# Optimization experiments

Hardware: AMD Instinct MI355X
Metric: run time of the kernel (lower is better)

## Reference

```python
import jax, jax.numpy as jnp
import numpy as np
import itertools

EPS = 1e-6
OUT = 1024            # out_size[0]
RRNG = (16.0, 16.0)   # local sampling region per column (rrange)


def setup_inputs() -> dict:
    key = jax.random.key(0)
    ks = jax.random.split(key, 6)
    b, n, c, g, rad, rank = 8, 4096, 32, 4, 4, 2
    k = n // c
    in_size = 1024
    rng = jnp.array([float(OUT), float(in_size)])
    # continuous index tuples, strictly inside [0, dim-1)
    means = jax.random.uniform(ks[0], (b, n, rank)) * (rng - 1.0)
    sigmas = jax.random.uniform(ks[1], (b, n, rank)) * 0.5 + 0.1
    values = jax.random.normal(ks[2], (b, n))
    x = jax.random.normal(ks[3], (b, in_size))
    sampled_u = jax.random.uniform(ks[4], (b, k, c, g, rank))
    rr_u = jax.random.uniform(ks[5], (b, k, c, rad, rank))
    return {"x": x, "means": means, "sigmas": sigmas, "values": values,
            "sampled_u": sampled_u, "rr_u": rr_u}


def _generate_integer_tuples(means, sampled_u, rr_u, rng, rrng):
    # means: (b,k,c,rank)
    b, k, c, rank = means.shape
    # floor/ceil combinatorics: itertools.product([True, False], repeat=rank)
    fm = jnp.asarray([[int(v) for v in bits]
                      for bits in itertools.product([True, False], repeat=rank)],
                     dtype=bool)                       # (2^rank, rank)
    m = means[:, :, :, None, :]                         # (b,k,c,1,rank)
    neighbor = jnp.where(fm[None, None, None], jnp.floor(m), jnp.ceil(m))
    neighbor = jnp.broadcast_to(neighbor, (b, k, c, 2 ** rank, rank)).astype(jnp.int32)
    # global uniform samples over the full index range
    sampled = jnp.floor(sampled_u * (1.0 - EPS) * rng).astype(jnp.int32)
    # local uniform samples in a window of size rrng around round(means)
    mns = jnp.round(means)[:, :, :, None, :]
    lower = mns - rrng * 0.5
    upper = mns + rrng * 0.5
    lower = jnp.where(lower < 0.0, 0.0, lower)
    lower = jnp.where(upper > rng, rng - rrng, lower)
    rr = jnp.floor(rr_u * (1.0 - EPS) * rrng + lower).astype(jnp.int32)
    allints = jnp.concatenate([neighbor, sampled, rr], axis=3)  # (b,k,c,L,rank)
    return allints.reshape(b, k, -1, rank)                      # l = c*L


def _densities(points, means, sigmas):
    # points: (b,k,l,rank)  means/sigmas: (b,k,c,rank) -> (b,k,l,c)
    inv = jnp.sqrt(1.0 / (EPS + sigmas))
    diff = (points[:, :, :, None, :] - means[:, :, None, :, :]) * inv[:, :, None, :, :]
    return jnp.exp(-0.5 * jnp.sum(diff * diff, axis=-1))


def _mark_dups(ids):
    # ids: (b,k,l) scalar-encoded tuples; True = later occurrence of a duplicate
    # within the same (b,k) chunk context. Stable sort keeps first occurrence.
    order = jnp.argsort(ids, axis=-1)
    s = jnp.take_along_axis(ids, order, axis=-1)
    dup_s = jnp.concatenate([jnp.zeros(s.shape[:-1] + (1,), dtype=bool),
                             s[..., 1:] == s[..., :-1]], axis=-1)
    inv = jnp.argsort(order, axis=-1)
    return jnp.take_along_axis(dup_s, inv, axis=-1)


def reference(x, means, sigmas, values, sampled_u, rr_u):
    b, n, rank = means.shape
    _, k, c, g, _ = sampled_u.shape
    in_size = x.shape[1]
    rng = jnp.array([OUT, in_size], dtype=x.dtype)
    rrng = jnp.array(RRNG, dtype=x.dtype)

    means = means.reshape(b, k, c, rank)
    sigmas = sigmas.reshape(b, k, c, rank)
    values = values.reshape(b, k, c)

    ints = _generate_integer_tuples(means, sampled_u, rr_u, rng, rrng)  # (b,k,l,rank)
    indfl = ints.astype(x.dtype)

    dups = _mark_dups(ints[..., 0] * in_size + ints[..., 1])            # (b,k,l)
    props = _densities(indfl, means, sigmas)                            # (b,k,l,c)
    props = jnp.where(dups[..., None], 0.0, props)
    props = props / jnp.sum(props, axis=2, keepdims=True)

    vals = jnp.sum(props * values[:, :, None, :], axis=3)               # (b,k,l)

    idx = ints.reshape(b, -1, rank)
    v = vals.reshape(b, -1)
    bidx = jnp.arange(b)[:, None]
    # sparse contraction: out[b, i0] += v * x[b, i1]
    contrib = v * x[bidx, idx[..., 1]]
    out = jnp.zeros((b, OUT), x.dtype).at[bidx, idx[..., 0]].add(contrib)
    return out
```

## Files before the change

### kernel.cpp

```cpp
#include <hip/hip_runtime.h>

#define CQ 32
#define KQ 128
#define NPTS 384
#define OUTN 1024
#define BQ 8
#define NACC (BQ * OUTN)
#define HSZ 1024
#define GPB 2
#define KB (KQ / GPB)
#define WS_NEED ((size_t)BQ * KB * OUTN * sizeof(float))

__global__ void zero_out(float* __restrict__ out) {
    int i = blockIdx.x * blockDim.x + threadIdx.x;
    if (i < NACC) out[i] = 0.0f;
}

__device__ __forceinline__ float wave_red_dpp(float v) {
#define DPPADD(ctrl)                                                              \
    {                                                                             \
        int t_ = __builtin_amdgcn_update_dpp(0, __float_as_int(v), (ctrl), 0xF,   \
                                             0xF, true);                          \
        v += __int_as_float(t_);                                                  \
    }
    DPPADD(0x111)
    DPPADD(0x112)
    DPPADD(0x114)
    DPPADD(0x118)
    DPPADD(0x142)
    DPPADD(0x143)
#undef DPPADD
    return v;
}

__global__ __launch_bounds__(NPTS) void sparse_part(
    const float* __restrict__ x,
    const float* __restrict__ means,
    const float* __restrict__ sigmas,
    const float* __restrict__ values,
    const float* __restrict__ su,
    const float* __restrict__ ru,
    float* __restrict__ dst,
    int use_ws)
{
    const int kb = blockIdx.x, b = blockIdx.y;
    const int tid = threadIdx.x;
    const int lane = tid & 63, wid = tid >> 6;

    __shared__ float m0s[CQ], m1s[CQ], i0s[CQ], i1s[CQ], valc[CQ];
    __shared__ int htab[HSZ];
    __shared__ float part[6][CQ];
    __shared__ float wnorm[CQ];
    __shared__ float acc[OUTN];

    if (use_ws) {
        for (int i = tid; i < OUTN; i += NPTS) acc[i] = 0.0f;
    }

    const int c = tid / 12, j = tid % 12;
    const float CEPS = (float)(1.0 - 1e-6);

    for (int g = 0; g < GPB; ++g) {
        const int k = kb * GPB + g;
        const int gk = b * KQ + k;

        for (int i = tid; i < HSZ; i += NPTS) htab[i] = -1;
        if (tid < CQ) {
            int cb = gk * CQ + tid;
            m0s[tid] = means[cb * 2 + 0];
            m1s[tid] = means[cb * 2 + 1];
            i0s[tid] = __fsqrt_rn(__fdiv_rn(1.0f, __fadd_rn(1e-6f, sigmas[cb * 2 + 0])));
            i1s[tid] = __fsqrt_rn(__fdiv_rn(1.0f, __fadd_rn(1e-6f, sigmas[cb * 2 + 1])));
            valc[tid] = values[cb];
        }
        __syncthreads();

        const int cb = gk * CQ + c;
        const float mm0 = m0s[c], mm1 = m1s[c];
        int p0, p1;
        if (j < 4) {
            p0 = (int)((j >= 2) ? ceilf(mm0) : floorf(mm0));
            p1 = (int)((j & 1) ? ceilf(mm1) : floorf(mm1));
        } else if (j < 8) {
            int ub = (cb * 4 + (j - 4)) * 2;
            float u0 = su[ub], u1 = su[ub + 1];
            p0 = (int)floorf(__fmul_rn(__fmul_rn(u0, CEPS), 1024.0f));
            p1 = (int)floorf(__fmul_rn(__fmul_rn(u1, CEPS), 1024.0f));
        } else {
            int ub = (cb * 4 + (j - 8)) * 2;
            float u0 = ru[ub], u1 = ru[ub + 1];
            float mn0 = rintf(mm0), mn1 = rintf(mm1);
            float lo0 = mn0 - 8.0f; if (lo0 < 0.0f) lo0 = 0.0f; if (mn0 + 8.0f > 1024.0f) lo0 = 1008.0f;
            float lo1 = mn1 - 8.0f; if (lo1 < 0.0f) lo1 = 0.0f; if (mn1 + 8.0f > 1024.0f) lo1 = 1008.0f;
            p0 = (int)floorf(__fadd_rn(__fmul_rn(__fmul_rn(u0, CEPS), 16.0f), lo0));
            p1 = (int)floorf(__fadd_rn(__fmul_rn(__fmul_rn(u1, CEPS), 16.0f), lo1));
        }

        const int myid = p0 * 1024 + p1;
        int slot = (int)(((unsigned)myid * 2654435761u) >> 22);
        bool dup = false;
        while (true) {
            int prev = atomicCAS(&htab[slot], -1, myid);
            if (prev == -1) break;
            if (prev == myid) { dup = true; break; }
            slot = (slot + 1) & (HSZ - 1);
        }

        const float pf0 = (float)p0, pf1 = (float)p1;
        float pr[CQ];
        #pragma unroll
        for (int cc = 0; cc < CQ; ++cc) {
            float d0 = (pf0 - m0s[cc]) * i0s[cc];
            float d1 = (pf1 - m1s[cc]) * i1s[cc];
            float e = __expf(-0.5f * (d0 * d0 + d1 * d1));
            pr[cc] = dup ? 0.0f : e;
        }

        #pragma unroll
        for (int cc = 0; cc < CQ; ++cc) {
            float v = wave_red_dpp(pr[cc]);
            if (lane == 63) part[wid][cc] = v;
        }
        __syncthreads();
        if (tid < CQ) {
            float s = 0.0f;
            #pragma unroll
            for (int w = 0; w < 6; ++w) s += part[w][tid];
            wnorm[tid] = valc[tid] / s;
        }
        __syncthreads();

        if (!dup) {
            float vals = 0.0f;
            #pragma unroll
            for (int cc = 0; cc < CQ; ++cc) vals += pr[cc] * wnorm[cc];
            int g1 = p1 < 0 ? 0 : (p1 > OUTN - 1 ? OUTN - 1 : p1);
            float contrib = vals * x[b * OUTN + g1];
            if (p0 >= 0 && p0 < OUTN) {
                if (use_ws) atomicAdd(&acc[p0], contrib);
                else        atomicAdd(&dst[b * OUTN + p0], contrib);
            }
        }
        __syncthreads();
    }

    if (use_ws) {
        float* w = dst + ((size_t)b * KB + kb) * OUTN;
        for (int i = tid; i < OUTN; i += NPTS) w[i] = acc[i];
    }
}

__global__ void reduce_ws(const float* __restrict__ ws, float* __restrict__ out) {
    int t = blockIdx.x * blockDim.x + threadIdx.x;
    if (t >= NACC) return;
    int b = t >> 10, cidx = t & (OUTN - 1);
    const float* p = ws + (size_t)b * KB * OUTN + cidx;
    float s0 = 0.0f, s1 = 0.0f, s2 = 0.0f, s3 = 0.0f;
    #pragma unroll
    for (int k = 0; k < KB; k += 4) {
        s0 += p[(size_t)(k + 0) * OUTN];
        s1 += p[(size_t)(k + 1) * OUTN];
        s2 += p[(size_t)(k + 2) * OUTN];
        s3 += p[(size_t)(k + 3) * OUTN];
    }
    out[t] = (s0 + s1) + (s2 + s3);
}

extern "C" void kernel_launch(void* const* d_in, const int* in_sizes, int n_in,
                              void* d_out, int out_size, void* d_ws, size_t ws_size,
                              hipStream_t stream) {
    const float* x      = (const float*)d_in[0];
    const float* means  = (const float*)d_in[1];
    const float* sigmas = (const float*)d_in[2];
    const float* values = (const float*)d_in[3];
    const float* su     = (const float*)d_in[4];
    const float* ru     = (const float*)d_in[5];
    float* out = (float*)d_out;
    float* ws  = (float*)d_ws;

    if (ws_size >= WS_NEED) {
        sparse_part<<<dim3(KB, BQ), dim3(NPTS), 0, stream>>>(
            x, means, sigmas, values, su, ru, ws, 1);
        reduce_ws<<<dim3((NACC + 127) / 128), dim3(128), 0, stream>>>(ws, out);
    } else {
        zero_out<<<dim3((NACC + 255) / 256), dim3(256), 0, stream>>>(out);
        sparse_part<<<dim3(KB, BQ), dim3(NPTS), 0, stream>>>(
            x, means, sigmas, values, su, ru, out, 0);
    }
}
```

Measured before the change: 91.86 us.

## Process one k-group per block and hoist global loads ahead of hash-table init

Each block now handles a single k-group instead of looping over two, doubling the grid to 1024 blocks. Global loads of means, sigmas, values and the sample tuples are issued at kernel start and overlap the hash-table and accumulator initialisation. Gaussian parameters are packed into a float4 in shared memory so each inner-loop iteration does one LDS read. The trade-off is a workspace twice as large, so the reduce kernel sums 128 partial rows per output instead of 64 and moves twice the data.

Measured after the change: 96.51 us. +5.1%, slower.

```diff
diff --git a/kernel.cpp b/kernel.cpp
--- a/kernel.cpp
+++ b/kernel.cpp
@@ -7,9 +7,7 @@
 #define BQ 8
 #define NACC (BQ * OUTN)
 #define HSZ 1024
-#define GPB 2
-#define KB (KQ / GPB)
-#define WS_NEED ((size_t)BQ * KB * OUTN * sizeof(float))
+#define WS_NEED ((size_t)BQ * KQ * OUTN * sizeof(float))
 
 __global__ void zero_out(float* __restrict__ out) {
     int i = blockIdx.x * blockDim.x + threadIdx.x;
@@ -43,109 +41,111 @@
     float* __restrict__ dst,
     int use_ws)
 {
-    const int kb = blockIdx.x, b = blockIdx.y;
+    const int k = blockIdx.x, b = blockIdx.y;
     const int tid = threadIdx.x;
     const int lane = tid & 63, wid = tid >> 6;
+    const int gk = b * KQ + k;
+    const int c = tid / 12, j = tid % 12;
+    const int cb = gk * CQ + c;
+    const float CEPS = (float)(1.0 - 1e-6);
 
-    __shared__ float m0s[CQ], m1s[CQ], i0s[CQ], i1s[CQ], valc[CQ];
+    __shared__ float4 gp[CQ];
+    __shared__ float valc[CQ];
     __shared__ int htab[HSZ];
     __shared__ float part[6][CQ];
     __shared__ float wnorm[CQ];
     __shared__ float acc[OUTN];
 
+    const float2 mcb = *(const float2*)&means[cb * 2];
+    float2 uu = make_float2(0.0f, 0.0f);
+    if (j >= 8)       uu = *(const float2*)&ru[(cb * 4 + (j - 8)) * 2];
+    else if (j >= 4)  uu = *(const float2*)&su[(cb * 4 + (j - 4)) * 2];
+    float2 mg, sg; float vv = 0.0f;
+    if (tid < CQ) {
+        int cbs = gk * CQ + tid;
+        mg = *(const float2*)&means[cbs * 2];
+        sg = *(const float2*)&sigmas[cbs * 2];
+        vv = values[cbs];
+    }
+
+    for (int i = tid; i < HSZ; i += NPTS) htab[i] = -1;
     if (use_ws) {
         for (int i = tid; i < OUTN; i += NPTS) acc[i] = 0.0f;
     }
+    if (tid < CQ) {
+        float i0 = __fsqrt_rn(__fdiv_rn(1.0f, __fadd_rn(1e-6f, sg.x)));
+        float i1 = __fsqrt_rn(__fdiv_rn(1.0f, __fadd_rn(1e-6f, sg.y)));
+        gp[tid] = make_float4(mg.x, mg.y, i0, i1);
+        valc[tid] = vv;
+    }
 
-    const int c = tid / 12, j = tid % 12;
-    const float CEPS = (float)(1.0 - 1e-6);
+    const float mm0 = mcb.x, mm1 = mcb.y;
+    int p0, p1;
+    if (j < 4) {
+        p0 = (int)((j >= 2) ? ceilf(mm0) : floorf(mm0));
+        p1 = (int)((j & 1) ? ceilf(mm1) : floorf(mm1));
+    } else if (j < 8) {
+        p0 = (int)floorf(__fmul_rn(__fmul_rn(uu.x, CEPS), 1024.0f));
+        p1 = (int)floorf(__fmul_rn(__fmul_rn(uu.y, CEPS), 1024.0f));
+    } else {
+        float mn0 = rintf(mm0), mn1 = rintf(mm1);
+        float lo0 = mn0 - 8.0f; if (lo0 < 0.0f) lo0 = 0.0f; if (mn0 + 8.0f > 1024.0f) lo0 = 1008.0f;
+        float lo1 = mn1 - 8.0f; if (lo1 < 0.0f) lo1 = 0.0f; if (mn1 + 8.0f > 1024.0f) lo1 = 1008.0f;
+        p0 = (int)floorf(__fadd_rn(__fmul_rn(__fmul_rn(uu.x, CEPS), 16.0f), lo0));
+        p1 = (int)floorf(__fadd_rn(__fmul_rn(__fmul_rn(uu.y, CEPS), 16.0f), lo1));
+    }
+    __syncthreads();
 
-    for (int g = 0; g < GPB; ++g) {
-        const int k = kb * GPB + g;
-        const int gk = b * KQ + k;
+    const int myid = p0 * 1024 + p1;
+    int slot = (int)(((unsigned)myid * 2654435761u) >> 22);
+    bool dup = false;
+    while (true) {
+        int prev = atomicCAS(&htab[slot], -1, myid);
+        if (prev == -1) break;
+        if (prev == myid) { dup = true; break; }
+        slot = (slot + 1) & (HSZ - 1);
+    }
 
-        for (int i = tid; i < HSZ; i += NPTS) htab[i] = -1;
-        if (tid < CQ) {
-            int cb = gk * CQ + tid;
-            m0s[tid] = means[cb * 2 + 0];
-            m1s[tid] = means[cb * 2 + 1];
-            i0s[tid] = __fsqrt_rn(__fdiv_rn(1.0f, __fadd_rn(1e-6f, sigmas[cb * 2 + 0])));
-            i1s[tid] = __fsqrt_rn(__fdiv_rn(1.0f, __fadd_rn(1e-6f, sigmas[cb * 2 + 1])));
-            valc[tid] = values[cb];
+    const float pf0 = (float)p0, pf1 = (float)p1;
+    float pr[CQ];
+    #pragma unroll
+    for (int cc = 0; cc < CQ; ++cc) {
+        float4 g = gp[cc];
+        float d0 = (pf0 - g.x) * g.z;
+        float d1 = (pf1 - g.y) * g.w;
+        float e = __expf(-0.5f * (d0 * d0 + d1 * d1));
+        pr[cc] = dup ? 0.0f : e;
+    }
+
+    #pragma unroll
+    for (int cc = 0; cc < CQ; ++cc) {
+        float v = wave_red_dpp(pr[cc]);
+        if (lane == 63) part[wid][cc] = v;
+    }
+    __syncthreads();
+    if (tid < CQ) {
+        float s = 0.0f;
+        #pragma unroll
+        for (int w = 0; w < 6; ++w) s += part[w][tid];
+        wnorm[tid] = valc[tid] / s;
+    }
+    __syncthreads();
+
+    if (!dup) {
+        float vals = 0.0f;
+        #pragma unroll
+        for (int cc = 0; cc < CQ; ++cc) vals += pr[cc] * wnorm[cc];
+        int g1 = p1 < 0 ? 0 : (p1 > OUTN - 1 ? OUTN - 1 : p1);
+        float contrib = vals * x[b * OUTN + g1];
+        if (p0 >= 0 && p0 < OUTN) {
+            if (use_ws) atomicAdd(&acc[p0], contrib);
+            else        atomicAdd(&dst[b * OUTN + p0], contrib);
         }
-        __syncthreads();
-
-        const int cb = gk * CQ + c;
-        const float mm0 = m0s[c], mm1 = m1s[c];
-        int p0, p1;
-        if (j < 4) {
-            p0 = (int)((j >= 2) ? ceilf(mm0) : floorf(mm0));
-            p1 = (int)((j & 1) ? ceilf(mm1) : floorf(mm1));
-        } else if (j < 8) {
-            int ub = (cb * 4 + (j - 4)) * 2;
-            float u0 = su[ub], u1 = su[ub + 1];
-            p0 = (int)floorf(__fmul_rn(__fmul_rn(u0, CEPS), 1024.0f));
-            p1 = (int)floorf(__fmul_rn(__fmul_rn(u1, CEPS), 1024.0f));
-        } else {
-            int ub = (cb * 4 + (j - 8)) * 2;
-            float u0 = ru[ub], u1 = ru[ub + 1];
-            float mn0 = rintf(mm0), mn1 = rintf(mm1);
-            float lo0 = mn0 - 8.0f; if (lo0 < 0.0f) lo0 = 0.0f; if (mn0 + 8.0f > 1024.0f) lo0 = 1008.0f;
-            float lo1 = mn1 - 8.0f; if (lo1 < 0.0f) lo1 = 0.0f; if (mn1 + 8.0f > 1024.0f) lo1 = 1008.0f;
-            p0 = (int)floorf(__fadd_rn(__fmul_rn(__fmul_rn(u0, CEPS), 16.0f), lo0));
-            p1 = (int)floorf(__fadd_rn(__fmul_rn(__fmul_rn(u1, CEPS), 16.0f), lo1));
-        }
-
-        const int myid = p0 * 1024 + p1;
-        int slot = (int)(((unsigned)myid * 2654435761u) >> 22);
-        bool dup = false;
-        while (true) {
-            int prev = atomicCAS(&htab[slot], -1, myid);
-            if (prev == -1) break;
-            if (prev == myid) { dup = true; break; }
-            slot = (slot + 1) & (HSZ - 1);
-        }
-
-        const float pf0 = (float)p0, pf1 = (float)p1;
-        float pr[CQ];
-        #pragma unroll
-        for (int cc = 0; cc < CQ; ++cc) {
-            float d0 = (pf0 - m0s[cc]) * i0s[cc];
-            float d1 = (pf1 - m1s[cc]) * i1s[cc];
-            float e = __expf(-0.5f * (d0 * d0 + d1 * d1));
-            pr[cc] = dup ? 0.0f : e;
-        }
-
-        #pragma unroll
-        for (int cc = 0; cc < CQ; ++cc) {
-            float v = wave_red_dpp(pr[cc]);
-            if (lane == 63) part[wid][cc] = v;
-        }
-        __syncthreads();
-        if (tid < CQ) {
-            float s = 0.0f;
-            #pragma unroll
-            for (int w = 0; w < 6; ++w) s += part[w][tid];
-            wnorm[tid] = valc[tid] / s;
-        }
-        __syncthreads();
-
-        if (!dup) {
-            float vals = 0.0f;
-            #pragma unroll
-            for (int cc = 0; cc < CQ; ++cc) vals += pr[cc] * wnorm[cc];
-            int g1 = p1 < 0 ? 0 : (p1 > OUTN - 1 ? OUTN - 1 : p1);
-            float contrib = vals * x[b * OUTN + g1];
-            if (p0 >= 0 && p0 < OUTN) {
-                if (use_ws) atomicAdd(&acc[p0], contrib);
-                else        atomicAdd(&dst[b * OUTN + p0], contrib);
-            }
-        }
-        __syncthreads();
     }
 
     if (use_ws) {
-        float* w = dst + ((size_t)b * KB + kb) * OUTN;
+        __syncthreads();
+        float* w = dst + (size_t)gk * OUTN;
         for (int i = tid; i < OUTN; i += NPTS) w[i] = acc[i];
     }
 }
@@ -154,10 +154,10 @@
     int t = blockIdx.x * blockDim.x + threadIdx.x;
     if (t >= NACC) return;
     int b = t >> 10, cidx = t & (OUTN - 1);
-    const float* p = ws + (size_t)b * KB * OUTN + cidx;
+    const float* p = ws + (size_t)b * KQ * OUTN + cidx;
     float s0 = 0.0f, s1 = 0.0f, s2 = 0.0f, s3 = 0.0f;
     #pragma unroll
-    for (int k = 0; k < KB; k += 4) {
+    for (int k = 0; k < KQ; k += 4) {
         s0 += p[(size_t)(k + 0) * OUTN];
         s1 += p[(size_t)(k + 1) * OUTN];
         s2 += p[(size_t)(k + 2) * OUTN];
@@ -179,12 +179,12 @@
     float* ws  = (float*)d_ws;
 
     if (ws_size >= WS_NEED) {
-        sparse_part<<<dim3(KB, BQ), dim3(NPTS), 0, stream>>>(
+        sparse_part<<<dim3(KQ, BQ), dim3(NPTS), 0, stream>>>(
             x, means, sigmas, values, su, ru, ws, 1);
         reduce_ws<<<dim3((NACC + 127) / 128), dim3(128), 0, stream>>>(ws, out);
     } else {
         zero_out<<<dim3((NACC + 255) / 256), dim3(256), 0, stream>>>(out);
-        sparse_part<<<dim3(KB, BQ), dim3(NPTS), 0, stream>>>(
+        sparse_part<<<dim3(KQ, BQ), dim3(NPTS), 0, stream>>>(
             x, means, sigmas, values, su, ru, out, 0);
     }
 }
```
